# Optimization experiments

Measured on AMD Instinct MI355X. Metric: run time of the kernel, lower is better.

Reference implementation:

```python
import jax, jax.numpy as jnp
import numpy as np

# Dimensions (see shape_source): B batches, W walks, L walk length, N anonymized node-id space
B, W, L, N = 256, 128, 20, 64
SIGMA = 2.0  # CooccurrenceMatrix(sigma=2.0)


def setup_inputs() -> dict:
    key = jax.random.key(0)
    k1, k2 = jax.random.split(key)
    anonymized_nodes = jax.random.randint(k1, (B, W, L), 0, N, dtype=jnp.int32)
    walk_masks = jax.random.randint(k2, (B, W, L), 0, 2).astype(bool)
    # Gaussian positional kernel buffer: kernel[i,j] = exp(-(i-j)^2 / sigma^2)
    pos = jnp.arange(L, dtype=jnp.float32)
    kernel = jnp.exp(-((pos[:, None] - pos[None, :]) ** 2) / (SIGMA ** 2))
    return {"anonymized_nodes": anonymized_nodes, "walk_masks": walk_masks, "kernel": kernel}


def reference(anonymized_nodes, walk_masks, kernel):
    # Faithful vectorized form of CooccurrenceMatrix.forward.
    # Original: per batch, group valid (walk,pos) entries by node id (sort +
    # change-points); for each group with >=2 entries, scatter-add
    # kernel[pos_i, pos_j] into cooccurrence[b, walk_i, walk_j] for all pairs
    # (i,j) in the group (including i==j). Then normalize by outer product of
    # walk lengths, clamp, tanh.
    valid = walk_masks.astype(jnp.float32)                     # [B,W,L]
    # T[b,w,l,n] = 1 if entry (w,l) is valid and holds node id n
    T = jax.nn.one_hot(anonymized_nodes, N, dtype=jnp.float32) * valid[..., None]  # [B,W,L,N]
    # Segments with < 2 occurrences contribute nothing (original skips them)
    cnt = T.sum(axis=(1, 2))                                   # [B,N]
    T = T * (cnt >= 2.0).astype(jnp.float32)[:, None, None, :]
    K = jnp.clip(kernel, -10.0, 10.0)                          # clamp as in _add_segment_deterministic
    # cooccurrence[b,w,v] = sum_n sum_{l,m} T[b,w,l,n] K[l,m] T[b,v,m,n]
    S = jnp.einsum('bwln,lm->bwmn', T, K)                      # [B,W,L,N]
    cooc = jnp.einsum('bwmn,bvmn->bwv', S, T)                  # [B,W,W]
    # Normalization by walk-length outer product
    walk_lens = valid.sum(-1)                                  # [B,W]
    norm = jnp.clip(walk_lens[:, :, None] * walk_lens[:, None, :], 1e-6, None)
    valid_pairs = (walk_lens[:, :, None] > 0) & (walk_lens[:, None, :] > 0)
    cooc = jnp.where(valid_pairs, cooc / norm, 0.0)
    return jnp.tanh(jnp.clip(cooc, -10.0, 10.0))
```

## Files before the change

kernel.cpp:

```cpp
#include <hip/hip_runtime.h>
#include <hip/hip_bf16.h>

#define BB   256
#define W    128
#define L    20
#define NN   64
#define WL   (W * L)
#define NT   1024
#define CS   129
#define NSLOT 3

__global__ __launch_bounds__(NT) void cooc_kernel(
    const int* __restrict__ nodes,
    const void* __restrict__ masks,
    const float* __restrict__ kern,
    float* __restrict__ out)
{
    __shared__ __align__(16) float cooc[W * CS];
    __shared__ unsigned short ent[WL];
    __shared__ __align__(16) float Ks[L * L];
    __shared__ int cnt[NN];
    __shared__ int cur[NN];
    __shared__ int eIncl[NN];
    __shared__ int wlen[W];
    __shared__ int det[3];

    const int tid = threadIdx.x;
    const int b = blockIdx.x;
    const int base = b * WL;

    if (tid < 3) det[tid] = 0;
    if (tid < NN) cnt[tid] = 0;
    if (tid < W) wlen[tid] = 0;
    if (tid < L * L) {
        float k = kern[tid];
        Ks[tid] = fminf(fmaxf(k, -10.f), 10.f);
    }
    {
        float4* c4 = (float4*)cooc;
        for (int i = tid; i < (W * CS) / 4; i += NT)
            c4[i] = make_float4(0.f, 0.f, 0.f, 0.f);
    }
    __syncthreads();

    {
        const unsigned* mi = (const unsigned*)masks;
        unsigned v = mi[tid];
        if (v > 1u) atomicOr(&det[0], 1);
        if (v != 0u && v != 0x3F800000u) atomicOr(&det[1], 1);
        if (v != 0u && v != 0x3F80u && v != 0x3F800000u && v != 0x3F803F80u &&
            v != 0x3C00u && v != 0x3C000000u && v != 0x3C003C00u)
            atomicOr(&det[2], 1);
    }
    __syncthreads();
    const int flag = det[0] ? (det[1] ? (det[2] ? 1 : 3) : 2) : 0;

    auto validAt = [&](int idx) -> bool {
        switch (flag) {
            case 0:  return ((const int*)masks)[idx] != 0;
            case 2:  return ((const float*)masks)[idx] != 0.0f;
            case 3:  return ((const unsigned short*)masks)[idx] != 0;
            default: return ((const unsigned char*)masks)[idx] != 0;
        }
    };

    int nreg[NSLOT];
    int wlreg[NSLOT];
    #pragma unroll
    for (int k = 0; k < NSLOT; k++) {
        int e = tid + k * NT;
        nreg[k] = -1;
        wlreg[k] = 0;
        if (e < WL && validAt(base + e)) {
            int n = nodes[base + e] & (NN - 1);
            int w = e / L;
            int l = e - w * L;
            nreg[k] = n;
            wlreg[k] = (w << 5) | l;
            atomicAdd(&cnt[n], 1);
            atomicAdd(&wlen[w], 1);
        }
    }
    __syncthreads();

    if (tid < NN) {
        int c = cnt[tid];
        int s = c;
        #pragma unroll
        for (int d = 1; d < NN; d <<= 1) {
            int t = __shfl_up(s, d, 64);
            if (tid >= d) s += t;
        }
        eIncl[tid] = s;
        cur[tid] = s - c;
    }
    __syncthreads();

    int posr[NSLOT], endr[NSLOT];
    #pragma unroll
    for (int k = 0; k < NSLOT; k++) {
        posr[k] = 0; endr[k] = 0;
        int n = nreg[k];
        if (n >= 0) {
            int p = atomicAdd(&cur[n], 1);
            ent[p] = (unsigned short)wlreg[k];
            if (cnt[n] >= 2) {
                posr[k] = p;
                endr[k] = eIncl[n];
                int w = wlreg[k] >> 5;
                atomicAdd(&cooc[w * CS + w], 0.5f);
            }
        }
    }
    __syncthreads();

    #pragma unroll
    for (int k = 0; k < NSLOT; k++) {
        const int p = posr[k], pe = endr[k];
        if (pe == 0) continue;
        const int w1row = (wlreg[k] >> 5) * CS;
        const int l1base = (wlreg[k] & 31) * L;
        #pragma unroll 4
        for (int j = p + 1; j < pe; j++) {
            int e2 = ent[j];
            atomicAdd(&cooc[w1row + (e2 >> 5)], Ks[l1base + (e2 & 31)]);
        }
    }
    __syncthreads();

    for (int i = tid; i < W * W; i += NT) {
        int wr = i >> 7;
        int v = i & (W - 1);
        int lw = wlen[wr], lv = wlen[v];
        float o = 0.f;
        if (lw > 0 && lv > 0) {
            float s = cooc[wr * CS + v] + cooc[v * CS + wr];
            float nrm = fmaxf((float)lw * (float)lv, 1e-6f);
            float x = s / nrm;
            x = fminf(fmaxf(x, -10.f), 10.f);
            o = tanhf(x);
        }
        out[b * W * W + i] = o;
    }
}

extern "C" void kernel_launch(void* const* d_in, const int* in_sizes, int n_in,
                              void* d_out, int out_size, void* d_ws, size_t ws_size,
                              hipStream_t stream) {
    const int*   nodes = (const int*)d_in[0];
    const void*  masks = d_in[1];
    const float* kern  = (const float*)d_in[2];
    float* out = (float*)d_out;

    cooc_kernel<<<BB, NT, 0, stream>>>(nodes, masks, kern, out);
}
```

Measured before the change: 93.96 us.

## Balance pair scatter with cyclic half-pairs and vectorize normalization epilogue

Each entry in a node group now handles half of the group's pairs in cyclic order and scatter-adds symmetrically into both cooc[w1][w2] and cooc[w2][w1]. Previously the first entries in a group did most of the upper-triangle work, so load across threads was uneven. The final pass then reads the full symmetric matrix with float4 loads and uses a fast exp2/rcp tanh instead of summing transposed entries, with the row stride padded to 132 for alignment. The mask word load is hoisted and one barrier is dropped. The trade-off is twice as many atomics per pair and a less precise tanh approximation.

```diff
diff --git a/kernel.cpp b/kernel.cpp
--- a/kernel.cpp
+++ b/kernel.cpp
@@ -7,7 +7,7 @@
 #define NN   64
 #define WL   (W * L)
 #define NT   1024
-#define CS   129
+#define CS   132
 #define NSLOT 3
 
 __global__ __launch_bounds__(NT) void cooc_kernel(
@@ -22,12 +22,14 @@
     __shared__ int cnt[NN];
     __shared__ int cur[NN];
     __shared__ int eIncl[NN];
-    __shared__ int wlen[W];
+    __shared__ __align__(16) int wlen[W];
     __shared__ int det[3];
 
     const int tid = threadIdx.x;
     const int b = blockIdx.x;
     const int base = b * WL;
+
+    const unsigned mword = ((const unsigned*)masks)[tid];
 
     if (tid < 3) det[tid] = 0;
     if (tid < NN) cnt[tid] = 0;
@@ -41,11 +43,8 @@
         for (int i = tid; i < (W * CS) / 4; i += NT)
             c4[i] = make_float4(0.f, 0.f, 0.f, 0.f);
     }
-    __syncthreads();
-
     {
-        const unsigned* mi = (const unsigned*)masks;
-        unsigned v = mi[tid];
+        unsigned v = mword;
         if (v > 1u) atomicOr(&det[0], 1);
         if (v != 0u && v != 0x3F800000u) atomicOr(&det[1], 1);
         if (v != 0u && v != 0x3F80u && v != 0x3F800000u && v != 0x3F803F80u &&
@@ -96,19 +95,22 @@
     }
     __syncthreads();
 
-    int posr[NSLOT], endr[NSLOT];
+    int qr[NSLOT], cr[NSLOT], bsr[NSLOT];
     #pragma unroll
     for (int k = 0; k < NSLOT; k++) {
-        posr[k] = 0; endr[k] = 0;
+        qr[k] = 0; cr[k] = 0; bsr[k] = 0;
         int n = nreg[k];
         if (n >= 0) {
             int p = atomicAdd(&cur[n], 1);
             ent[p] = (unsigned short)wlreg[k];
-            if (cnt[n] >= 2) {
-                posr[k] = p;
-                endr[k] = eIncl[n];
+            int c = cnt[n];
+            if (c >= 2) {
+                int bs = eIncl[n] - c;
+                qr[k] = p - bs;
+                cr[k] = c;
+                bsr[k] = bs;
                 int w = wlreg[k] >> 5;
-                atomicAdd(&cooc[w * CS + w], 0.5f);
+                atomicAdd(&cooc[w * CS + w], 1.0f);
             }
         }
     }
@@ -116,31 +118,54 @@
 
     #pragma unroll
     for (int k = 0; k < NSLOT; k++) {
-        const int p = posr[k], pe = endr[k];
-        if (pe == 0) continue;
+        const int c = cr[k];
+        if (c < 2) continue;
+        const int q = qr[k], bs = bsr[k];
         const int w1row = (wlreg[k] >> 5) * CS;
+        const int w1 = wlreg[k] >> 5;
         const int l1base = (wlreg[k] & 31) * L;
+        const int hd = (c - 1) >> 1;
         #pragma unroll 4
-        for (int j = p + 1; j < pe; j++) {
-            int e2 = ent[j];
-            atomicAdd(&cooc[w1row + (e2 >> 5)], Ks[l1base + (e2 & 31)]);
+        for (int d = 1; d <= hd; d++) {
+            int j = q + d;
+            if (j >= c) j -= c;
+            int e2 = ent[bs + j];
+            int w2 = e2 >> 5;
+            float kv = Ks[l1base + (e2 & 31)];
+            atomicAdd(&cooc[w1row + w2], kv);
+            atomicAdd(&cooc[w2 * CS + w1], kv);
+        }
+        if ((c & 1) == 0 && q < (c >> 1)) {
+            int j = q + (c >> 1);
+            int e2 = ent[bs + j];
+            int w2 = e2 >> 5;
+            float kv = Ks[l1base + (e2 & 31)];
+            atomicAdd(&cooc[w1row + w2], kv);
+            atomicAdd(&cooc[w2 * CS + w1], kv);
         }
     }
     __syncthreads();
 
-    for (int i = tid; i < W * W; i += NT) {
+    for (int s = 0; s < (W * W) / (NT * 4); s++) {
+        int i = (tid + s * NT) * 4;
         int wr = i >> 7;
         int v = i & (W - 1);
-        int lw = wlen[wr], lv = wlen[v];
-        float o = 0.f;
-        if (lw > 0 && lv > 0) {
-            float s = cooc[wr * CS + v] + cooc[v * CS + wr];
-            float nrm = fmaxf((float)lw * (float)lv, 1e-6f);
-            float x = s / nrm;
+        float4 hv = *(const float4*)&cooc[wr * CS + v];
+        int4  lv4 = *(const int4*)&wlen[v];
+        int   lw  = wlen[wr];
+        float r[4] = {hv.x, hv.y, hv.z, hv.w};
+        int   lv[4] = {lv4.x, lv4.y, lv4.z, lv4.w};
+        float o[4];
+        #pragma unroll
+        for (int u = 0; u < 4; u++) {
+            float nrm = (float)(lw * lv[u]);
+            float x = r[u] * __builtin_amdgcn_rcpf(fmaxf(nrm, 1e-6f));
             x = fminf(fmaxf(x, -10.f), 10.f);
-            o = tanhf(x);
+            float e = __builtin_amdgcn_exp2f(x * 2.885390082f);
+            float t = (e - 1.f) * __builtin_amdgcn_rcpf(e + 1.f);
+            o[u] = (lw > 0 && lv[u] > 0) ? t : 0.f;
         }
-        out[b * W * W + i] = o;
+        *(float4*)&out[b * W * W + i] = make_float4(o[0], o[1], o[2], o[3]);
     }
 }
 
```

Measured after the change: 108.3 us. 15.3% more time.
